# Optimization experiments

Measured on AMD Instinct MI355X. Metric: run time of the kernel, lower is better.

The kernel has to match this reference:

```python
import jax, jax.numpy as jnp
import numpy as np

B, T, C, H = 2, 2048, 1024, 16
HD = C // H  # head size = 64
EPS = 1e-5


def setup_inputs() -> dict:
    key = jax.random.key(0)
    ks = jax.random.split(key, 16)
    s = 0.02
    return {
        "x": jax.random.normal(ks[0], (B, T, C), jnp.float32),
        # per-head q/k/v projections, stacked: [H, C, HD]
        "Wq": jax.random.normal(ks[1], (H, C, HD), jnp.float32) * s,
        "Wk": jax.random.normal(ks[2], (H, C, HD), jnp.float32) * s,
        "Wv": jax.random.normal(ks[3], (H, C, HD), jnp.float32) * s,
        "Wproj": jax.random.normal(ks[4], (C, C), jnp.float32) * s,
        "bproj": jnp.zeros((C,), jnp.float32),
        "W1": jax.random.normal(ks[5], (C, 4 * C), jnp.float32) * s,
        "b1": jnp.zeros((4 * C,), jnp.float32),
        "W2": jax.random.normal(ks[6], (4 * C, C), jnp.float32) * s,
        "b2": jnp.zeros((C,), jnp.float32),
        "g1": jnp.ones((C,), jnp.float32),
        "be1": jnp.zeros((C,), jnp.float32),
        "g2": jnp.ones((C,), jnp.float32),
        "be2": jnp.zeros((C,), jnp.float32),
    }


def _layernorm(x, g, b):
    mu = jnp.mean(x, axis=-1, keepdims=True)
    var = jnp.mean(jnp.square(x - mu), axis=-1, keepdims=True)
    return (x - mu) * jax.lax.rsqrt(var + EPS) * g + b


def _block(x, Wq, Wk, Wv, Wproj, bproj, W1, b1, W2, b2, g1, be1, g2, be2):
    Bx, Tx, Cx = x.shape
    h = _layernorm(x, g1, be1)
    q = jnp.einsum("btc,hcd->bhtd", h, Wq)
    k = jnp.einsum("btc,hcd->bhtd", h, Wk)
    v = jnp.einsum("btc,hcd->bhtd", h, Wv)
    scores = jnp.einsum("bhtd,bhsd->bhts", q, k) * (HD ** -0.5)  # [B,H,T,T]
    causal = jnp.tril(jnp.ones((Tx, Tx), bool))
    scores = jnp.where(causal, scores, -jnp.inf)
    w = jax.nn.softmax(scores, axis=-1)
    o = jnp.einsum("bhts,bhsd->bhtd", w, v)
    o = o.transpose(0, 2, 1, 3).reshape(Bx, Tx, Cx)  # concat heads
    x = x + o @ Wproj + bproj
    h2 = _layernorm(x, g2, be2)
    ff = jax.nn.relu(h2 @ W1 + b1) @ W2 + b2
    return x + ff


def reference(x, Wq, Wk, Wv, Wproj, bproj, W1, b1, W2, b2, g1, be1, g2, be2):
    return _block(x, Wq, Wk, Wv, Wproj, bproj, W1, b1, W2, b2, g1, be1, g2, be2)
```

## Files before the change

kernel.cpp:

```cpp
#include <hip/hip_runtime.h>
#include <stdint.h>


typedef unsigned short u16;
typedef unsigned int u32;
typedef __attribute__((ext_vector_type(4))) float f32x4;
typedef __attribute__((ext_vector_type(8))) short s16x8;

__device__ __forceinline__ u16 f2bf(float f) {
  u32 u = __builtin_bit_cast(u32, f);
  u += 0x7fffu + ((u >> 16) & 1u);
  return (u16)(u >> 16);
}
__device__ __forceinline__ s16x8 ld_s16x8_a8(const u16* p) {
  union { uint2 d[2]; s16x8 v; } u;
  u.d[0] = *(const uint2*)p;
  u.d[1] = *(const uint2*)(p + 4);
  return u.v;
}
__device__ __forceinline__ void gload16(const u16* g, u16* lds_base) {
  __builtin_amdgcn_global_load_lds(
      (const __attribute__((address_space(1))) void*)g,
      (__attribute__((address_space(3))) void*)lds_base, 16, 0, 0);
}

__global__ __launch_bounds__(256) void transpose_f32_bf16(
    const float* __restrict__ src, u16* __restrict__ dst,
    int Ccols, long srcZ, long dstZ, int dstStride) {
  __shared__ float t[64][65];
  const float* s = src + (size_t)blockIdx.z * srcZ;
  u16* d = dst + (size_t)blockIdx.z * dstZ;
  const int r0 = blockIdx.y * 64, c0 = blockIdx.x * 64;
  const int tr = threadIdx.x >> 4, tc4 = (threadIdx.x & 15) * 4;
#pragma unroll
  for (int p = 0; p < 4; ++p) {
    int r = p * 16 + tr;
    float4 v = *(const float4*)(s + (size_t)(r0 + r) * Ccols + c0 + tc4);
    t[r][tc4 + 0] = v.x; t[r][tc4 + 1] = v.y;
    t[r][tc4 + 2] = v.z; t[r][tc4 + 3] = v.w;
  }
  __syncthreads();
#pragma unroll
  for (int p = 0; p < 4; ++p) {
    int c = p * 16 + tr;
    uint2 pk;
    pk.x = (u32)f2bf(t[tc4 + 0][c]) | ((u32)f2bf(t[tc4 + 1][c]) << 16);
    pk.y = (u32)f2bf(t[tc4 + 2][c]) | ((u32)f2bf(t[tc4 + 3][c]) << 16);
    *(uint2*)(d + (size_t)(c0 + c) * dstStride + r0 + tc4) = pk;
  }
}

__global__ __launch_bounds__(256) void ln_kernel(
    const float* __restrict__ x, const float* __restrict__ g,
    const float* __restrict__ be, u16* __restrict__ out) {
  const int row = blockIdx.x, tid = threadIdx.x;
  const float* xr = x + (size_t)row * 1024;
  float4 v = *(const float4*)(xr + tid * 4);
  float s = v.x + v.y + v.z + v.w;
  float q = v.x * v.x + v.y * v.y + v.z * v.z + v.w * v.w;
#pragma unroll
  for (int off = 32; off > 0; off >>= 1) {
    s += __shfl_down(s, off);
    q += __shfl_down(q, off);
  }
  __shared__ float red[8];
  const int wid = tid >> 6, lane = tid & 63;
  if (lane == 0) { red[wid] = s; red[wid + 4] = q; }
  __syncthreads();
  s = red[0] + red[1] + red[2] + red[3];
  q = red[4] + red[5] + red[6] + red[7];
  const float mu = s * (1.f / 1024.f);
  const float var = q * (1.f / 1024.f) - mu * mu;
  const float rs = rsqrtf(var + 1e-5f);
  float4 gv = *(const float4*)(g + tid * 4);
  float4 bv = *(const float4*)(be + tid * 4);
  float o0 = (v.x - mu) * rs * gv.x + bv.x;
  float o1 = (v.y - mu) * rs * gv.y + bv.y;
  float o2 = (v.z - mu) * rs * gv.z + bv.z;
  float o3 = (v.w - mu) * rs * gv.w + bv.w;
  uint2 pk;
  pk.x = (u32)f2bf(o0) | ((u32)f2bf(o1) << 16);
  pk.y = (u32)f2bf(o2) | ((u32)f2bf(o3) << 16);
  *(uint2*)(out + (size_t)row * 1024 + tid * 4) = pk;
}

template <int EPI, int BM>
__global__ __launch_bounds__(256) void gemm_kernel(
    const u16* __restrict__ A, const u16* __restrict__ BT,
    const float* __restrict__ bias, const float* __restrict__ resid,
    void* __restrict__ out, int M, int N, int K) {
  __shared__ u16 sA[BM][64];
  __shared__ u16 sB[128][64];
  const int tid = threadIdx.x;
  const int m0 = blockIdx.y * BM, n0 = blockIdx.x * 128;
  const int wid = tid >> 6, lane = tid & 63;
  const int wr = (wid >> 1) * (BM / 2), wc = (wid & 1) * 64;
  const int l15 = lane & 15, g = lane >> 4;
  constexpr int MR = BM / 32;
  f32x4 acc[MR][4] = {};
  const int lr = lane >> 3;
  const int cswz = ((lane & 7) * 8) ^ (lr << 3);

  for (int k0 = 0; k0 < K; k0 += 64) {
    __syncthreads();
#pragma unroll
    for (int p = 0; p < MR; ++p) {
      const int row = (p * 4 + wid) * 8 + lr;
      gload16(A + (size_t)(m0 + row) * K + k0 + cswz, &sA[(p * 4 + wid) * 8][0]);
    }
#pragma unroll
    for (int p = 0; p < 4; ++p) {
      const int row = (p * 4 + wid) * 8 + lr;
      gload16(BT + (size_t)(n0 + row) * K + k0 + cswz, &sB[(p * 4 + wid) * 8][0]);
    }
    __syncthreads();
#pragma unroll
    for (int kk = 0; kk < 64; kk += 32) {
      s16x8 af[MR], bf[4];
#pragma unroll
      for (int m = 0; m < MR; ++m) {
        const int R = wr + m * 16 + l15;
        af[m] = *(const s16x8*)(&sA[R][(kk + g * 8) ^ ((R & 7) << 3)]);
      }
#pragma unroll
      for (int n = 0; n < 4; ++n) {
        const int R = wc + n * 16 + l15;
        bf[n] = *(const s16x8*)(&sB[R][(kk + g * 8) ^ ((R & 7) << 3)]);
      }
#pragma unroll
      for (int m = 0; m < MR; ++m)
#pragma unroll
        for (int n = 0; n < 4; ++n)
          acc[m][n] = __builtin_amdgcn_mfma_f32_16x16x32_bf16(af[m], bf[n], acc[m][n], 0, 0, 0);
    }
  }

#pragma unroll
  for (int m = 0; m < MR; ++m) {
#pragma unroll
    for (int n = 0; n < 4; ++n) {
      const int col = n0 + wc + n * 16 + l15;
      float bv = 0.f;
      if (EPI >= 1) bv = bias[col];
#pragma unroll
      for (int i = 0; i < 4; ++i) {
        const int row = m0 + wr + m * 16 + g * 4 + i;
        float v = acc[m][n][i];
        if (EPI >= 1) v += bv;
        if (EPI == 1) v = fmaxf(v, 0.f);
        if (EPI == 2) {
          v += resid[(size_t)row * N + col];
          ((float*)out)[(size_t)row * N + col] = v;
        } else {
          ((u16*)out)[(size_t)row * N + col] = f2bf(v);
        }
      }
    }
  }
}

__global__ __launch_bounds__(256) void attn_mfma_kernel(
    const u16* __restrict__ qkv, u16* __restrict__ o) {
  __shared__ u16 sK[64][72];
  __shared__ u16 sVt[64][68];
  __shared__ u16 sP[4][16][72];
  const int tid = threadIdx.x;
  const int b = blockIdx.y >> 4, h = blockIdx.y & 15;
  const int w = tid >> 6, lane = tid & 63;
  const int l15 = lane & 15, g = lane >> 4;
  const float c = 0.125f * 1.4426950408889634f;
  const int ks_r = tid >> 2, ks_c = (tid & 3) * 16;
  const int vs_s = tid & 63, vs_d = (tid >> 6) * 8;
  const u16* kbase = qkv + (size_t)(b * 2048) * 3072 + 1024 + h * 64;
  const u16* vbase = kbase + 1024;

#pragma unroll 1
  for (int pass = 0; pass < 2; ++pass) {
    const int qb = pass == 0 ? (31 - (int)blockIdx.x) : (int)blockIdx.x;

    const size_t qrow = (size_t)(b * 2048 + qb * 64 + w * 16 + l15);
    s16x8 qf0 = *(const s16x8*)(qkv + qrow * 3072 + h * 64 + g * 8);
    s16x8 qf1 = *(const s16x8*)(qkv + qrow * 3072 + h * 64 + 32 + g * 8);

    f32x4 oacc[4] = {};
    float mrow[4] = {-1e30f, -1e30f, -1e30f, -1e30f};
    float lrow[4] = {0.f, 0.f, 0.f, 0.f};

    const int nt = qb + 1;
    uint4 kr0, kr1, vr0, vr1;
    {
      const u16* kp = kbase + (size_t)(ks_r)*3072 + ks_c;
      kr0 = *(const uint4*)kp; kr1 = *(const uint4*)(kp + 8);
      const u16* vp = vbase + (size_t)(vs_s)*3072 + vs_d;
      vr0 = *(const uint4*)vp; vr1 = *(const uint4*)(vp + 32);
    }
    for (int t = 0; t < nt; ++t) {
      __syncthreads();
      *(uint4*)(&sK[ks_r][ks_c]) = kr0;
      *(uint4*)(&sK[ks_r][ks_c + 8]) = kr1;
      {
        union { uint4 q4; u16 e[8]; } va, vb;
        va.q4 = vr0; vb.q4 = vr1;
#pragma unroll
        for (int j = 0; j < 8; ++j) sVt[vs_d + j][vs_s] = va.e[j];
#pragma unroll
        for (int j = 0; j < 8; ++j) sVt[vs_d + 32 + j][vs_s] = vb.e[j];
      }
      __syncthreads();
      if (t + 1 < nt) {
        const u16* kp = kbase + (size_t)((t + 1) * 64 + ks_r) * 3072 + ks_c;
        kr0 = *(const uint4*)kp; kr1 = *(const uint4*)(kp + 8);
        const u16* vp = vbase + (size_t)((t + 1) * 64 + vs_s) * 3072 + vs_d;
        vr0 = *(const uint4*)vp; vr1 = *(const uint4*)(vp + 32);
      }

      f32x4 st[4];
#pragma unroll
      for (int n = 0; n < 4; ++n) {
        s16x8 k0 = *(const s16x8*)(&sK[n * 16 + l15][g * 8]);
        s16x8 k1 = *(const s16x8*)(&sK[n * 16 + l15][32 + g * 8]);
        f32x4 a = {};
        a = __builtin_amdgcn_mfma_f32_16x16x32_bf16(qf0, k0, a, 0, 0, 0);
        a = __builtin_amdgcn_mfma_f32_16x16x32_bf16(qf1, k1, a, 0, 0, 0);
        st[n] = a;
      }
      if (t == qb) {
#pragma unroll
        for (int n = 0; n < 4; ++n)
#pragma unroll
          for (int i = 0; i < 4; ++i) {
            const int srel = n * 16 + l15, qrel = w * 16 + 4 * g + i;
            if (srel > qrel) st[n][i] = -1e30f;
          }
      }
      float pm[4];
#pragma unroll
      for (int i = 0; i < 4; ++i)
        pm[i] = fmaxf(fmaxf(st[0][i], st[1][i]), fmaxf(st[2][i], st[3][i]));
#pragma unroll
      for (int msk = 1; msk < 16; msk <<= 1)
#pragma unroll
        for (int i = 0; i < 4; ++i) pm[i] = fmaxf(pm[i], __shfl_xor(pm[i], msk));
      float corr[4];
#pragma unroll
      for (int i = 0; i < 4; ++i) {
        const float mnew = fmaxf(mrow[i], pm[i]);
        corr[i] = exp2f((mrow[i] - mnew) * c);
        mrow[i] = mnew;
        lrow[i] *= corr[i];
      }
#pragma unroll
      for (int dt = 0; dt < 4; ++dt)
#pragma unroll
        for (int i = 0; i < 4; ++i) oacc[dt][i] *= corr[i];
      float p[4][4];
#pragma unroll
      for (int n = 0; n < 4; ++n)
#pragma unroll
        for (int i = 0; i < 4; ++i) p[n][i] = exp2f((st[n][i] - mrow[i]) * c);
#pragma unroll
      for (int i = 0; i < 4; ++i)
        lrow[i] += (p[0][i] + p[1][i]) + (p[2][i] + p[3][i]);
#pragma unroll
      for (int n = 0; n < 4; ++n)
#pragma unroll
        for (int i = 0; i < 4; ++i)
          sP[w][4 * g + i][n * 16 + l15] = f2bf(p[n][i]);
      s16x8 pf0 = *(const s16x8*)(&sP[w][l15][g * 8]);
      s16x8 pf1 = *(const s16x8*)(&sP[w][l15][32 + g * 8]);
#pragma unroll
      for (int dt = 0; dt < 4; ++dt) {
        s16x8 vf0 = ld_s16x8_a8(&sVt[dt * 16 + l15][g * 8]);
        s16x8 vf1 = ld_s16x8_a8(&sVt[dt * 16 + l15][32 + g * 8]);
        oacc[dt] = __builtin_amdgcn_mfma_f32_16x16x32_bf16(pf0, vf0, oacc[dt], 0, 0, 0);
        oacc[dt] = __builtin_amdgcn_mfma_f32_16x16x32_bf16(pf1, vf1, oacc[dt], 0, 0, 0);
      }
    }

#pragma unroll
    for (int msk = 1; msk < 16; msk <<= 1)
#pragma unroll
      for (int i = 0; i < 4; ++i) lrow[i] += __shfl_xor(lrow[i], msk);
    float inv[4];
#pragma unroll
    for (int i = 0; i < 4; ++i) inv[i] = 1.f / lrow[i];
#pragma unroll
    for (int dt = 0; dt < 4; ++dt)
#pragma unroll
      for (int i = 0; i < 4; ++i) {
        const size_t row = (size_t)(b * 2048 + qb * 64 + w * 16 + 4 * g + i);
        o[row * 1024 + h * 64 + dt * 16 + l15] = f2bf(oacc[dt][i] * inv[i]);
      }
  }
}

extern "C" void kernel_launch(void* const* d_in, const int* in_sizes, int n_in,
                              void* d_out, int out_size, void* d_ws, size_t ws_size,
                              hipStream_t stream) {
  const float* x     = (const float*)d_in[0];
  const float* Wq    = (const float*)d_in[1];
  const float* Wk    = (const float*)d_in[2];
  const float* Wv    = (const float*)d_in[3];
  const float* Wproj = (const float*)d_in[4];
  const float* bproj = (const float*)d_in[5];
  const float* W1    = (const float*)d_in[6];
  const float* b1    = (const float*)d_in[7];
  const float* W2    = (const float*)d_in[8];
  const float* b2    = (const float*)d_in[9];
  const float* g1    = (const float*)d_in[10];
  const float* be1   = (const float*)d_in[11];
  const float* g2    = (const float*)d_in[12];
  const float* be2   = (const float*)d_in[13];
  float* out = (float*)d_out;

  u16* WqkvT  = (u16*)d_ws;
  u16* WprojT = WqkvT + (size_t)3072 * 1024;
  u16* W1T    = WprojT + (size_t)1024 * 1024;
  u16* W2T    = W1T + (size_t)4096 * 1024;
  u16* hbuf   = W2T + (size_t)1024 * 4096;
  u16* qkv    = hbuf + (size_t)4096 * 1024;
  u16* obuf   = qkv + (size_t)4096 * 3072;
  float* x2   = (float*)(obuf + (size_t)4096 * 1024);
  u16* a1     = (u16*)(x2 + (size_t)4096 * 1024);

  transpose_f32_bf16<<<dim3(1, 16, 16), 256, 0, stream>>>(Wq, WqkvT,                      64, 65536, 65536, 1024);
  transpose_f32_bf16<<<dim3(1, 16, 16), 256, 0, stream>>>(Wk, WqkvT + (size_t)1024 * 1024, 64, 65536, 65536, 1024);
  transpose_f32_bf16<<<dim3(1, 16, 16), 256, 0, stream>>>(Wv, WqkvT + (size_t)2048 * 1024, 64, 65536, 65536, 1024);
  transpose_f32_bf16<<<dim3(16, 16, 1), 256, 0, stream>>>(Wproj, WprojT, 1024, 0, 0, 1024);
  transpose_f32_bf16<<<dim3(64, 16, 1), 256, 0, stream>>>(W1, W1T, 4096, 0, 0, 1024);
  transpose_f32_bf16<<<dim3(16, 64, 1), 256, 0, stream>>>(W2, W2T, 1024, 0, 0, 4096);

  ln_kernel<<<4096, 256, 0, stream>>>(x, g1, be1, hbuf);
  gemm_kernel<0, 128><<<dim3(24, 32), 256, 0, stream>>>(hbuf, WqkvT, nullptr, nullptr, qkv, 4096, 3072, 1024);
  attn_mfma_kernel<<<dim3(16, 32), 256, 0, stream>>>(qkv, obuf);
  gemm_kernel<2, 64><<<dim3(8, 64), 256, 0, stream>>>(obuf, WprojT, bproj, x, x2, 4096, 1024, 1024);
  ln_kernel<<<4096, 256, 0, stream>>>(x2, g2, be2, hbuf);
  gemm_kernel<1, 128><<<dim3(32, 32), 256, 0, stream>>>(hbuf, W1T, b1, nullptr, a1, 4096, 4096, 1024);
  gemm_kernel<2, 64><<<dim3(8, 64), 256, 0, stream>>>(a1, W2T, b2, x2, out, 4096, 1024, 4096);
}
```

Baseline: 279.7 us.

## Widen attention query tile to 128 rows with lazy softmax rescaling

```diff
diff --git a/kernel.cpp b/kernel.cpp
--- a/kernel.cpp
+++ b/kernel.cpp
@@ -163,7 +163,7 @@
     const u16* __restrict__ qkv, u16* __restrict__ o) {
   __shared__ u16 sK[64][72];
   __shared__ u16 sVt[64][68];
-  __shared__ u16 sP[4][16][72];
+  __shared__ u16 sP[4][32][72];
   const int tid = threadIdx.x;
   const int b = blockIdx.y >> 4, h = blockIdx.y & 15;
   const int w = tid >> 6, lane = tid & 63;
@@ -173,125 +173,165 @@
   const int vs_s = tid & 63, vs_d = (tid >> 6) * 8;
   const u16* kbase = qkv + (size_t)(b * 2048) * 3072 + 1024 + h * 64;
   const u16* vbase = kbase + 1024;
-
-#pragma unroll 1
-  for (int pass = 0; pass < 2; ++pass) {
-    const int qb = pass == 0 ? (31 - (int)blockIdx.x) : (int)blockIdx.x;
-
-    const size_t qrow = (size_t)(b * 2048 + qb * 64 + w * 16 + l15);
-    s16x8 qf0 = *(const s16x8*)(qkv + qrow * 3072 + h * 64 + g * 8);
-    s16x8 qf1 = *(const s16x8*)(qkv + qrow * 3072 + h * 64 + 32 + g * 8);
-
-    f32x4 oacc[4] = {};
-    float mrow[4] = {-1e30f, -1e30f, -1e30f, -1e30f};
-    float lrow[4] = {0.f, 0.f, 0.f, 0.f};
-
-    const int nt = qb + 1;
-    uint4 kr0, kr1, vr0, vr1;
+  const int qb = 15 - (int)blockIdx.x;
+  const int qw = qb * 128 + w * 32;
+
+  s16x8 qf[2][2];
+#pragma unroll
+  for (int mt = 0; mt < 2; ++mt) {
+    const size_t qrow = (size_t)(b * 2048 + qw + mt * 16 + l15);
+    qf[mt][0] = *(const s16x8*)(qkv + qrow * 3072 + h * 64 + g * 8);
+    qf[mt][1] = *(const s16x8*)(qkv + qrow * 3072 + h * 64 + 32 + g * 8);
+  }
+
+  f32x4 oacc[2][4] = {};
+  float mrow[2][4], lrow[2][4];
+#pragma unroll
+  for (int mt = 0; mt < 2; ++mt)
+#pragma unroll
+    for (int i = 0; i < 4; ++i) { mrow[mt][i] = -1e30f; lrow[mt][i] = 0.f; }
+
+  const int nt = 2 * qb + 2;
+  uint4 kr0, kr1, vr0, vr1;
+  {
+    const u16* kp = kbase + (size_t)(ks_r)*3072 + ks_c;
+    kr0 = *(const uint4*)kp; kr1 = *(const uint4*)(kp + 8);
+    const u16* vp = vbase + (size_t)(vs_s)*3072 + vs_d;
+    vr0 = *(const uint4*)vp; vr1 = *(const uint4*)(vp + 32);
+  }
+  for (int t = 0; t < nt; ++t) {
+    __syncthreads();
+    *(uint4*)(&sK[ks_r][ks_c]) = kr0;
+    *(uint4*)(&sK[ks_r][ks_c + 8]) = kr1;
     {
-      const u16* kp = kbase + (size_t)(ks_r)*3072 + ks_c;
+      union { uint4 q4; u16 e[8]; } va, vb;
+      va.q4 = vr0; vb.q4 = vr1;
+#pragma unroll
+      for (int j = 0; j < 8; ++j) sVt[vs_d + j][vs_s] = va.e[j];
+#pragma unroll
+      for (int j = 0; j < 8; ++j) sVt[vs_d + 32 + j][vs_s] = vb.e[j];
+    }
+    __syncthreads();
+    if (t + 1 < nt) {
+      const u16* kp = kbase + (size_t)((t + 1) * 64 + ks_r) * 3072 + ks_c;
       kr0 = *(const uint4*)kp; kr1 = *(const uint4*)(kp + 8);
-      const u16* vp = vbase + (size_t)(vs_s)*3072 + vs_d;
+      const u16* vp = vbase + (size_t)((t + 1) * 64 + vs_s) * 3072 + vs_d;
       vr0 = *(const uint4*)vp; vr1 = *(const uint4*)(vp + 32);
     }
-    for (int t = 0; t < nt; ++t) {
-      __syncthreads();
-      *(uint4*)(&sK[ks_r][ks_c]) = kr0;
-      *(uint4*)(&sK[ks_r][ks_c + 8]) = kr1;
-      {
-        union { uint4 q4; u16 e[8]; } va, vb;
-        va.q4 = vr0; vb.q4 = vr1;
-#pragma unroll
-        for (int j = 0; j < 8; ++j) sVt[vs_d + j][vs_s] = va.e[j];
-#pragma unroll
-        for (int j = 0; j < 8; ++j) sVt[vs_d + 32 + j][vs_s] = vb.e[j];
-      }
-      __syncthreads();
-      if (t + 1 < nt) {
-        const u16* kp = kbase + (size_t)((t + 1) * 64 + ks_r) * 3072 + ks_c;
-        kr0 = *(const uint4*)kp; kr1 = *(const uint4*)(kp + 8);
-        const u16* vp = vbase + (size_t)((t + 1) * 64 + vs_s) * 3072 + vs_d;
-        vr0 = *(const uint4*)vp; vr1 = *(const uint4*)(vp + 32);
-      }
-
-      f32x4 st[4];
-#pragma unroll
-      for (int n = 0; n < 4; ++n) {
-        s16x8 k0 = *(const s16x8*)(&sK[n * 16 + l15][g * 8]);
-        s16x8 k1 = *(const s16x8*)(&sK[n * 16 + l15][32 + g * 8]);
+
+    f32x4 st[2][4];
+    __builtin_amdgcn_s_setprio(1);
+#pragma unroll
+    for (int n = 0; n < 4; ++n) {
+      s16x8 k0 = *(const s16x8*)(&sK[n * 16 + l15][g * 8]);
+      s16x8 k1 = *(const s16x8*)(&sK[n * 16 + l15][32 + g * 8]);
+#pragma unroll
+      for (int mt = 0; mt < 2; ++mt) {
         f32x4 a = {};
-        a = __builtin_amdgcn_mfma_f32_16x16x32_bf16(qf0, k0, a, 0, 0, 0);
-        a = __builtin_amdgcn_mfma_f32_16x16x32_bf16(qf1, k1, a, 0, 0, 0);
-        st[n] = a;
-      }
-      if (t == qb) {
+        a = __builtin_amdgcn_mfma_f32_16x16x32_bf16(qf[mt][0], k0, a, 0, 0, 0);
+        a = __builtin_amdgcn_mfma_f32_16x16x32_bf16(qf[mt][1], k1, a, 0, 0, 0);
+        st[mt][n] = a;
+      }
+    }
+    __builtin_amdgcn_s_setprio(0);
+    if (t >= 2 * qb) {
+#pragma unroll
+      for (int mt = 0; mt < 2; ++mt)
 #pragma unroll
         for (int n = 0; n < 4; ++n)
 #pragma unroll
           for (int i = 0; i < 4; ++i) {
-            const int srel = n * 16 + l15, qrel = w * 16 + 4 * g + i;
-            if (srel > qrel) st[n][i] = -1e30f;
+            const int s_abs = t * 64 + n * 16 + l15;
+            const int q_abs = qw + mt * 16 + 4 * g + i;
+            if (s_abs > q_abs) st[mt][n][i] = -1e30f;
           }
-      }
-      float pm[4];
+    }
+    float pm[2][4];
+#pragma unroll
+    for (int mt = 0; mt < 2; ++mt)
 #pragma unroll
       for (int i = 0; i < 4; ++i)
-        pm[i] = fmaxf(fmaxf(st[0][i], st[1][i]), fmaxf(st[2][i], st[3][i]));
-#pragma unroll
-      for (int msk = 1; msk < 16; msk <<= 1)
-#pragma unroll
-        for (int i = 0; i < 4; ++i) pm[i] = fmaxf(pm[i], __shfl_xor(pm[i], msk));
-      float corr[4];
-#pragma unroll
-      for (int i = 0; i < 4; ++i) {
-        const float mnew = fmaxf(mrow[i], pm[i]);
-        corr[i] = exp2f((mrow[i] - mnew) * c);
-        mrow[i] = mnew;
-        lrow[i] *= corr[i];
-      }
+        pm[mt][i] = fmaxf(fmaxf(st[mt][0][i], st[mt][1][i]),
+                          fmaxf(st[mt][2][i], st[mt][3][i]));
+#pragma unroll
+    for (int msk = 1; msk < 16; msk <<= 1)
+#pragma unroll
+      for (int mt = 0; mt < 2; ++mt)
+#pragma unroll
+        for (int i = 0; i < 4; ++i) pm[mt][i] = fmaxf(pm[mt][i], __shfl_xor(pm[mt][i], msk));
+    bool need = false;
+#pragma unroll
+    for (int mt = 0; mt < 2; ++mt)
+#pragma unroll
+      for (int i = 0; i < 4; ++i) need = need || (pm[mt][i] > mrow[mt][i] + 16.f);
+    if (__any(need)) {
+#pragma unroll
+      for (int mt = 0; mt < 2; ++mt)
+#pragma unroll
+        for (int i = 0; i < 4; ++i) {
+          const float mnew = fmaxf(mrow[mt][i], pm[mt][i]);
+          const float corr = exp2f((mrow[mt][i] - mnew) * c);
+          mrow[mt][i] = mnew;
+          lrow[mt][i] *= corr;
+#pragma unroll
+          for (int dt = 0; dt < 4; ++dt) oacc[mt][dt][i] *= corr;
+        }
+    }
+#pragma unroll
+    for (int mt = 0; mt < 2; ++mt)
+#pragma unroll
+      for (int n = 0; n < 4; ++n)
+#pragma unroll
+        for (int i = 0; i < 4; ++i)
+          st[mt][n][i] = exp2f((st[mt][n][i] - mrow[mt][i]) * c);
+#pragma unroll
+    for (int mt = 0; mt < 2; ++mt)
+#pragma unroll
+      for (int i = 0; i < 4; ++i)
+        lrow[mt][i] += (st[mt][0][i] + st[mt][1][i]) + (st[mt][2][i] + st[mt][3][i]);
+#pragma unroll
+    for (int mt = 0; mt < 2; ++mt)
+#pragma unroll
+      for (int n = 0; n < 4; ++n)
+#pragma unroll
+        for (int i = 0; i < 4; ++i)
+          sP[w][mt * 16 + 4 * g + i][n * 16 + l15] = f2bf(st[mt][n][i]);
+    s16x8 pf[2][2];
+#pragma unroll
+    for (int mt = 0; mt < 2; ++mt) {
+      pf[mt][0] = *(const s16x8*)(&sP[w][mt * 16 + l15][g * 8]);
+      pf[mt][1] = *(const s16x8*)(&sP[w][mt * 16 + l15][32 + g * 8]);
+    }
+    __builtin_amdgcn_s_setprio(1);
+#pragma unroll
+    for (int dt = 0; dt < 4; ++dt) {
+      s16x8 vf0 = ld_s16x8_a8(&sVt[dt * 16 + l15][g * 8]);
+      s16x8 vf1 = ld_s16x8_a8(&sVt[dt * 16 + l15][32 + g * 8]);
+#pragma unroll
+      for (int mt = 0; mt < 2; ++mt) {
+        oacc[mt][dt] = __builtin_amdgcn_mfma_f32_16x16x32_bf16(pf[mt][0], vf0, oacc[mt][dt], 0, 0, 0);
+        oacc[mt][dt] = __builtin_amdgcn_mfma_f32_16x16x32_bf16(pf[mt][1], vf1, oacc[mt][dt], 0, 0, 0);
+      }
+    }
+    __builtin_amdgcn_s_setprio(0);
+  }
+
+#pragma unroll
+  for (int msk = 1; msk < 16; msk <<= 1)
+#pragma unroll
+    for (int mt = 0; mt < 2; ++mt)
+#pragma unroll
+      for (int i = 0; i < 4; ++i) lrow[mt][i] += __shfl_xor(lrow[mt][i], msk);
+#pragma unroll
+  for (int mt = 0; mt < 2; ++mt)
+#pragma unroll
+    for (int i = 0; i < 4; ++i) {
+      const float inv = 1.f / lrow[mt][i];
+      const size_t row = (size_t)(b * 2048 + qw + mt * 16 + 4 * g + i);
 #pragma unroll
       for (int dt = 0; dt < 4; ++dt)
-#pragma unroll
-        for (int i = 0; i < 4; ++i) oacc[dt][i] *= corr[i];
-      float p[4][4];
-#pragma unroll
-      for (int n = 0; n < 4; ++n)
-#pragma unroll
-        for (int i = 0; i < 4; ++i) p[n][i] = exp2f((st[n][i] - mrow[i]) * c);
-#pragma unroll
-      for (int i = 0; i < 4; ++i)
-        lrow[i] += (p[0][i] + p[1][i]) + (p[2][i] + p[3][i]);
-#pragma unroll
-      for (int n = 0; n < 4; ++n)
-#pragma unroll
-        for (int i = 0; i < 4; ++i)
-          sP[w][4 * g + i][n * 16 + l15] = f2bf(p[n][i]);
-      s16x8 pf0 = *(const s16x8*)(&sP[w][l15][g * 8]);
-      s16x8 pf1 = *(const s16x8*)(&sP[w][l15][32 + g * 8]);
-#pragma unroll
-      for (int dt = 0; dt < 4; ++dt) {
-        s16x8 vf0 = ld_s16x8_a8(&sVt[dt * 16 + l15][g * 8]);
-        s16x8 vf1 = ld_s16x8_a8(&sVt[dt * 16 + l15][32 + g * 8]);
-        oacc[dt] = __builtin_amdgcn_mfma_f32_16x16x32_bf16(pf0, vf0, oacc[dt], 0, 0, 0);
-        oacc[dt] = __builtin_amdgcn_mfma_f32_16x16x32_bf16(pf1, vf1, oacc[dt], 0, 0, 0);
-      }
-    }
-
-#pragma unroll
-    for (int msk = 1; msk < 16; msk <<= 1)
-#pragma unroll
-      for (int i = 0; i < 4; ++i) lrow[i] += __shfl_xor(lrow[i], msk);
-    float inv[4];
-#pragma unroll
-    for (int i = 0; i < 4; ++i) inv[i] = 1.f / lrow[i];
-#pragma unroll
-    for (int dt = 0; dt < 4; ++dt)
-#pragma unroll
-      for (int i = 0; i < 4; ++i) {
-        const size_t row = (size_t)(b * 2048 + qb * 64 + w * 16 + 4 * g + i);
-        o[row * 1024 + h * 64 + dt * 16 + l15] = f2bf(oacc[dt][i] * inv[i]);
-      }
-  }
+        o[row * 1024 + h * 64 + dt * 16 + l15] = f2bf(oacc[mt][dt][i] * inv);
+    }
 }
 
 extern "C" void kernel_launch(void* const* d_in, const int* in_sizes, int n_in,
```

After: 310.4 us. 10.9% more time.

## Add 256x256-tile 8-wave GEMM with direct-to-LDS double buffering for FFN1

Applied to the files above, without the earlier changes.

```diff
diff --git a/kernel.cpp b/kernel.cpp
--- a/kernel.cpp
+++ b/kernel.cpp
@@ -159,6 +159,146 @@
   }
 }
 
+template <int EPI>
+__global__ __launch_bounds__(512, 2) void gemm256_kernel(
+    const u16* __restrict__ A, const u16* __restrict__ BT,
+    const float* __restrict__ bias, const float* __restrict__ resid,
+    void* __restrict__ out, int M, int N, int K) {
+  __shared__ u16 lds[2][2][256][64];
+  const int tid = threadIdx.x;
+  const int wid = tid >> 6, lane = tid & 63;
+  const int m0 = blockIdx.y * 256, n0 = blockIdx.x * 256;
+  const int wr = (wid >> 2) * 128;
+  const int wc = (wid & 3) * 64;
+  const int l15 = lane & 15, g = lane >> 4;
+  const int lr = lane >> 3;
+  const int cswz = ((lane & 7) * 8) ^ (lr << 3);
+  const int swz = (l15 & 7) << 3;
+  const u16* Abase = A + (size_t)m0 * K;
+  const u16* Bbase = BT + (size_t)n0 * K;
+  const int nkt = K >> 6;
+
+  f32x4 acc[8][4] = {};
+  s16x8 bf[4][2];
+
+  auto issue_half = [&](const u16* Xbase, int xi, int t, int hf) {
+    const int b = t & 1;
+    const int r0 = hf * 128 + wid * 8;
+    gload16(Xbase + (size_t)(r0 + lr) * K + t * 64 + cswz, &lds[b][xi][r0][0]);
+    gload16(Xbase + (size_t)(r0 + 64 + lr) * K + t * 64 + cswz, &lds[b][xi][r0 + 64][0]);
+  };
+
+  issue_half(Abase, 0, 0, 0);
+  issue_half(Abase, 0, 0, 1);
+  issue_half(Bbase, 1, 0, 0);
+  issue_half(Bbase, 1, 0, 1);
+  asm volatile("s_waitcnt vmcnt(0)" ::: "memory");
+  __builtin_amdgcn_s_barrier();
+
+  for (int i = 0; i < nkt; i += 2) {
+#pragma unroll
+    for (int p = 0; p < 4; ++p) {
+      s16x8 af[2][2];
+#pragma unroll
+      for (int q = 0; q < 2; ++q) {
+        const int R = wr + (2 * p + q) * 16 + l15;
+#pragma unroll
+        for (int h = 0; h < 2; ++h)
+          af[q][h] = *(const s16x8*)(&lds[0][0][R][(h * 32 + g * 8) ^ swz]);
+      }
+      if (p == 0) {
+#pragma unroll
+        for (int n = 0; n < 4; ++n) {
+          const int R = wc + n * 16 + l15;
+#pragma unroll
+          for (int h = 0; h < 2; ++h)
+            bf[n][h] = *(const s16x8*)(&lds[0][1][R][(h * 32 + g * 8) ^ swz]);
+        }
+      }
+      if (i + 1 < nkt) {
+        if (p == 0) issue_half(Abase, 0, i + 1, 0);
+        else if (p == 1) issue_half(Abase, 0, i + 1, 1);
+        else if (p == 2) issue_half(Bbase, 1, i + 1, 0);
+        else issue_half(Bbase, 1, i + 1, 1);
+      }
+      __builtin_amdgcn_s_barrier();
+      asm volatile("s_waitcnt lgkmcnt(0)" ::: "memory");
+      __builtin_amdgcn_sched_barrier(0);
+      __builtin_amdgcn_s_setprio(1);
+#pragma unroll
+      for (int q = 0; q < 2; ++q)
+#pragma unroll
+        for (int n = 0; n < 4; ++n) {
+          acc[2 * p + q][n] = __builtin_amdgcn_mfma_f32_16x16x32_bf16(af[q][0], bf[n][0], acc[2 * p + q][n], 0, 0, 0);
+          acc[2 * p + q][n] = __builtin_amdgcn_mfma_f32_16x16x32_bf16(af[q][1], bf[n][1], acc[2 * p + q][n], 0, 0, 0);
+        }
+      __builtin_amdgcn_s_setprio(0);
+      if (p == 3)
+        asm volatile("s_waitcnt vmcnt(0)" ::: "memory");
+      __builtin_amdgcn_s_barrier();
+    }
+    if (i + 1 < nkt) {
+#pragma unroll
+      for (int p = 0; p < 4; ++p) {
+        s16x8 af[2][2];
+#pragma unroll
+        for (int q = 0; q < 2; ++q) {
+          const int R = wr + (2 * p + q) * 16 + l15;
+#pragma unroll
+          for (int h = 0; h < 2; ++h)
+            af[q][h] = *(const s16x8*)(&lds[1][0][R][(h * 32 + g * 8) ^ swz]);
+        }
+        if (p == 0) {
+#pragma unroll
+          for (int n = 0; n < 4; ++n) {
+            const int R = wc + n * 16 + l15;
+#pragma unroll
+            for (int h = 0; h < 2; ++h)
+              bf[n][h] = *(const s16x8*)(&lds[1][1][R][(h * 32 + g * 8) ^ swz]);
+          }
+        }
+        if (i + 2 < nkt) {
+          if (p == 0) issue_half(Abase, 0, i + 2, 0);
+          else if (p == 1) issue_half(Abase, 0, i + 2, 1);
+          else if (p == 2) issue_half(Bbase, 1, i + 2, 0);
+          else issue_half(Bbase, 1, i + 2, 1);
+        }
+        __builtin_amdgcn_s_barrier();
+        asm volatile("s_waitcnt lgkmcnt(0)" ::: "memory");
+        __builtin_amdgcn_sched_barrier(0);
+        __builtin_amdgcn_s_setprio(1);
+#pragma unroll
+        for (int q = 0; q < 2; ++q)
+#pragma unroll
+          for (int n = 0; n < 4; ++n) {
+            acc[2 * p + q][n] = __builtin_amdgcn_mfma_f32_16x16x32_bf16(af[q][0], bf[n][0], acc[2 * p + q][n], 0, 0, 0);
+            acc[2 * p + q][n] = __builtin_amdgcn_mfma_f32_16x16x32_bf16(af[q][1], bf[n][1], acc[2 * p + q][n], 0, 0, 0);
+          }
+        __builtin_amdgcn_s_setprio(0);
+        if (p == 3)
+          asm volatile("s_waitcnt vmcnt(0)" ::: "memory");
+        __builtin_amdgcn_s_barrier();
+      }
+    }
+  }
+
+#pragma unroll
+  for (int mi = 0; mi < 8; ++mi)
+#pragma unroll
+    for (int n = 0; n < 4; ++n) {
+      const int col = n0 + wc + n * 16 + l15;
+      float bv = (EPI >= 1) ? bias[col] : 0.f;
+#pragma unroll
+      for (int ii = 0; ii < 4; ++ii) {
+        const int row = m0 + wr + mi * 16 + g * 4 + ii;
+        float v = acc[mi][n][ii];
+        if (EPI >= 1) v += bv;
+        if (EPI == 1) v = fmaxf(v, 0.f);
+        ((u16*)out)[(size_t)row * N + col] = f2bf(v);
+      }
+    }
+}
+
 __global__ __launch_bounds__(256) void attn_mfma_kernel(
     const u16* __restrict__ qkv, u16* __restrict__ o) {
   __shared__ u16 sK[64][72];
@@ -335,6 +475,6 @@
   attn_mfma_kernel<<<dim3(16, 32), 256, 0, stream>>>(qkv, obuf);
   gemm_kernel<2, 64><<<dim3(8, 64), 256, 0, stream>>>(obuf, WprojT, bproj, x, x2, 4096, 1024, 1024);
   ln_kernel<<<4096, 256, 0, stream>>>(x2, g2, be2, hbuf);
-  gemm_kernel<1, 128><<<dim3(32, 32), 256, 0, stream>>>(hbuf, W1T, b1, nullptr, a1, 4096, 4096, 1024);
+  gemm256_kernel<1><<<dim3(16, 16), 512, 0, stream>>>(hbuf, W1T, b1, nullptr, a1, 4096, 4096, 1024);
   gemm_kernel<2, 64><<<dim3(8, 64), 256, 0, stream>>>(a1, W2T, b2, x2, out, 4096, 1024, 4096);
 }
```

New measurement: 272.3 us. 2.7% less time.
